# Kernel optimization log

Measured on AMD Instinct MI355X. Metric: run time of the kernel, lower is better.

Reference implementation:

```python
import jax, jax.numpy as jnp
import numpy as np

B, S, HID = 2, 4096, 2048
H, D = 16, 128
BS = 64            # block_size
SR = 0.5           # sparsity_ratio
NB = S // BS       # number of diagonal blocks
SCALE = D ** -0.5


def setup_inputs() -> dict:
    key = jax.random.key(0)
    ks = jax.random.split(key, 7)
    s = 0.02
    return {
        "hidden_states": jax.random.normal(ks[0], (B, S, HID), jnp.float32),
        "Wq": jax.random.normal(ks[1], (HID, H * D), jnp.float32) * s,
        "Wk": jax.random.normal(ks[2], (HID, H * D), jnp.float32) * s,
        "Wv": jax.random.normal(ks[3], (HID, H * D), jnp.float32) * s,
        "Wo": jax.random.normal(ks[4], (H * D, HID), jnp.float32) * s,
        "Wr": jax.random.normal(ks[5], (HID, H), jnp.float32) * s,   # block_router weight
        "br": jax.random.normal(ks[6], (H,), jnp.float32) * s,       # block_router bias
    }


def reference(hidden_states, Wq, Wk, Wv, Wo, Wr, br):
    # projections: torch Linear(x) == x @ W^T; weights stored pre-transposed here
    q = (hidden_states @ Wq).reshape(B, S, H, D).transpose(0, 2, 1, 3)  # [B,H,S,D]
    k = (hidden_states @ Wk).reshape(B, S, H, D).transpose(0, 2, 1, 3)
    v = (hidden_states @ Wv).reshape(B, S, H, D).transpose(0, 2, 1, 3)

    # per-head routing score, mean-pooled over batch (as in torch: routing_scores[:, h].mean())
    routing = jax.nn.sigmoid(hidden_states.mean(axis=1) @ Wr + br)      # [B,H]
    head_score = routing.mean(axis=0)                                   # [H]
    eff_sparsity = SR * (1.0 - head_score * 0.5)
    # torch: max(1, int(block_size * eff)); positive -> floor == int truncation
    attend_count = jnp.maximum(1, jnp.floor(BS * eff_sparsity).astype(jnp.int32))  # [H]

    # block-diagonal attention: only within-block scores are ever finite, so we
    # never materialize the full SxS matrix (softmax over -inf elsewhere is a no-op)
    qb = q.reshape(B, H, NB, BS, D)
    kb = k.reshape(B, H, NB, BS, D)
    vb = v.reshape(B, H, NB, BS, D)
    scores = jnp.einsum("bhnqd,bhnkd->bhnqk", qb, kb) * SCALE           # [B,H,NB,BS,BS]

    # rank of each key within its row (descending); keep == variable-k top-k mask.
    order = jnp.argsort(-scores, axis=-1)
    rank = jnp.argsort(order, axis=-1)
    keep = rank < attend_count[None, :, None, None, None]
    # non-top-k in-block entries are scattered as 0.0 (not -inf) in the original
    masked = jnp.where(keep, scores, 0.0)

    probs = jax.nn.softmax(masked.astype(jnp.float32), axis=-1).astype(q.dtype)
    out_b = jnp.einsum("bhnqk,bhnkd->bhnqd", probs, vb)                 # [B,H,NB,BS,D]
    out = out_b.reshape(B, H, S, D).transpose(0, 2, 1, 3).reshape(B, S, H * D)
    return out @ Wo
```

## Files before the change

### kernel.cpp

```cpp
#include <hip/hip_runtime.h>
#include <hip/hip_bf16.h>
#include <cstdint>
#include <cstddef>

#define B_   2
#define S_   4096
#define HIDN 2048
#define H_   16
#define D_   128
#define NB_  64
#define MTOT 8192
#define QKVN 6144
#define SCALE_ 0.08838834764831845f

typedef unsigned short ushort_t;
typedef __attribute__((ext_vector_type(8))) short short8;
typedef __attribute__((ext_vector_type(8))) ushort_t ushort8;
typedef __attribute__((ext_vector_type(4))) float f32x4;

__device__ inline float b2f(ushort_t x){ union{unsigned u; float f;} v; v.u=((unsigned)x)<<16; return v.f; }
__device__ inline ushort_t f2b(float f){ union{unsigned u; float f;} v; v.f=f; unsigned r=(v.u + 0x7FFF + ((v.u>>16)&1))>>16; return (ushort_t)r; }

#define MFMA_BF16(a,b,c) __builtin_amdgcn_mfma_f32_16x16x32_bf16((a),(b),(c),0,0,0)

__device__ inline void async16(const ushort_t* g, ushort_t* l){
  __builtin_amdgcn_global_load_lds(
      (const __attribute__((address_space(1))) void*)g,
      (__attribute__((address_space(3))) void*)l, 16, 0, 0);
}

__global__ void bsa_convpart(const float* __restrict__ hs, ushort_t* __restrict__ hsB,
                             float* __restrict__ part){
  int t = threadIdx.x;
  int c  = blockIdx.x*512 + t*2;
  int sc = blockIdx.y;
  int b  = blockIdx.z;
  const float* p = hs  + ((size_t)b*S_ + (size_t)sc*128)*HIDN + c;
  ushort_t*    q = hsB + ((size_t)b*S_ + (size_t)sc*128)*HIDN + c;
  float s0=0.f, s1=0.f;
  #pragma unroll 8
  for (int i=0;i<128;i++){
    float2 v = *(const float2*)(p + (size_t)i*HIDN);
    s0 += v.x; s1 += v.y;
    unsigned pk = (unsigned)f2b(v.x) | ((unsigned)f2b(v.y)<<16);
    *(unsigned*)(q + (size_t)i*HIDN) = pk;
  }
  part[((b*32+sc)*HIDN)+c]   = s0;
  part[((b*32+sc)*HIDN)+c+1] = s1;
}

__global__ void bsa_router(const float* __restrict__ part, const float* __restrict__ Wr,
                           const float* __restrict__ br, int* __restrict__ counts){
  __shared__ float cm[2*HIDN];
  __shared__ float sig[2*H_];
  int t = threadIdx.x;
  {
    int b  = t>>9;
    int c4 = (t&511)*4;
    float sx=0.f, sy=0.f, sz=0.f, sw=0.f;
    for (int j=0;j<32;j++){
      float4 v = *(const float4*)&part[((b*32+j)*HIDN)+c4];
      sx+=v.x; sy+=v.y; sz+=v.z; sw+=v.w;
    }
    cm[b*HIDN+c4+0]=sx*(1.0f/S_);
    cm[b*HIDN+c4+1]=sy*(1.0f/S_);
    cm[b*HIDN+c4+2]=sz*(1.0f/S_);
    cm[b*HIDN+c4+3]=sw*(1.0f/S_);
  }
  __syncthreads();
  if (t < 256){
    int g = t>>3;
    int sl = t&7;
    int b = g>>4, h = g&15;
    float acc = 0.f;
    for (int c=sl; c<HIDN; c+=8) acc += cm[b*HIDN+c]*Wr[c*H_+h];
    acc += __shfl_xor(acc, 4);
    acc += __shfl_xor(acc, 2);
    acc += __shfl_xor(acc, 1);
    if (sl==0) sig[g] = 1.f/(1.f+expf(-(acc + br[h])));
  }
  __syncthreads();
  if (t < H_){
    float score = 0.5f*(sig[t] + sig[H_+t]);
    float eff = 0.5f*(1.0f - score*0.5f);
    int ac = (int)floorf(64.f*eff);
    if (ac < 1) ac = 1;
    counts[t] = ac;
  }
}

__global__ void bsa_transpose(const float* w0, const float* w1, const float* w2, const float* w3,
                              ushort_t* o0, ushort_t* o1, ushort_t* o2, ushort_t* o3){
  const float* src; ushort_t* dst;
  switch(blockIdx.z){
    case 0: src=w0; dst=o0; break;
    case 1: src=w1; dst=o1; break;
    case 2: src=w2; dst=o2; break;
    default: src=w3; dst=o3; break;
  }
  __shared__ ushort_t tt[64*72];
  int t = threadIdx.x;
  int r0 = blockIdx.y*64, c0 = blockIdx.x*64;
  #pragma unroll
  for (int it=0; it<16; it++){
    int f = it*256 + t;
    int r = f>>6, c = f&63;
    tt[c*72 + (r ^ ((c&7)<<3))] = f2b(src[(size_t)(r0+r)*HIDN + (c0+c)]);
  }
  __syncthreads();
  #pragma unroll
  for (int it=0; it<2; it++){
    int f = it*256 + t;
    int cc = f>>3, rb = (f&7)<<3;
    ushort8 v = *(const ushort8*)&tt[cc*72 + (rb ^ ((cc&7)<<3))];
    *(ushort8*)&dst[(size_t)(c0+cc)*HIDN + r0 + rb] = v;
  }
}


#define SBAR asm volatile("s_barrier" ::: "memory")
#define WVM4 asm volatile("s_waitcnt vmcnt(4)" ::: "memory")
#define WVM2 asm volatile("s_waitcnt vmcnt(2)" ::: "memory")
#define WVM0 asm volatile("s_waitcnt vmcnt(0)" ::: "memory")
#define PHI  __builtin_amdgcn_s_setprio(1)
#define PLO  __builtin_amdgcn_s_setprio(0)

__device__ __forceinline__ short8 lds_frag(const ushort_t* buf, int row, int kb){
  int off = ((row<<7) + kb) ^ ((row&7)<<4);
  return *(const short8*)((const char*)buf + off);
}

__device__ __forceinline__ void rd_a(short8 (&a)[4][2], const ushort_t* buf, int r0, int l16, int quad){
  #pragma unroll
  for (int mi=0; mi<4; mi++)
    #pragma unroll
    for (int ks=0; ks<2; ks++)
      a[mi][ks] = lds_frag(buf, r0 + mi*16 + l16, ks*64 + quad*16);
}
__device__ __forceinline__ void rd_a2(short8 (&a)[4][2], const ushort_t* buf, int r0, int l16, int quad, int mi0){
  #pragma unroll
  for (int mi=mi0; mi<mi0+2; mi++)
    #pragma unroll
    for (int ks=0; ks<2; ks++)
      a[mi][ks] = lds_frag(buf, r0 + mi*16 + l16, ks*64 + quad*16);
}
__device__ __forceinline__ void rd_b(short8 (&b)[2][2], const ushort_t* buf, int r0, int l16, int quad){
  #pragma unroll
  for (int ni=0; ni<2; ni++)
    #pragma unroll
    for (int ks=0; ks<2; ks++)
      b[ni][ks] = lds_frag(buf, r0 + ni*16 + l16, ks*64 + quad*16);
}
__device__ __forceinline__ void mm8(f32x4 (&acc)[8][4], const short8 (&a)[4][2],
                                    const short8 (&b)[2][2], int mo, int no){
  #pragma unroll
  for (int mi=0; mi<4; mi++)
    #pragma unroll
    for (int ni=0; ni<2; ni++){
      acc[mo+mi][no+ni] = MFMA_BF16(a[mi][0], b[ni][0], acc[mo+mi][no+ni]);
      acc[mo+mi][no+ni] = MFMA_BF16(a[mi][1], b[ni][1], acc[mo+mi][no+ni]);
    }
}
__device__ __forceinline__ void mm8h(f32x4 (&acc)[8][4], const short8 (&a)[4][2],
                                     const short8 (&b)[2][2], int mo, int no, int mi0){
  #pragma unroll
  for (int mi=mi0; mi<mi0+2; mi++)
    #pragma unroll
    for (int ni=0; ni<2; ni++){
      acc[mo+mi][no+ni] = MFMA_BF16(a[mi][0], b[ni][0], acc[mo+mi][no+ni]);
      acc[mo+mi][no+ni] = MFMA_BF16(a[mi][1], b[ni][1], acc[mo+mi][no+ni]);
    }
}
__device__ __forceinline__ void stage_half(ushort_t* ldsHalf, const ushort_t* g,
                                           int K, int w, int roff, int coff){
  async16(g + (size_t)(w*16 + roff)*K + coff,     ldsHalf + (w*2+0)*512);
  async16(g + (size_t)(w*16 + 8 + roff)*K + coff, ldsHalf + (w*2+1)*512);
}

template<int F32OUT>
__global__ __launch_bounds__(512, 2) void bsa_gemm8(const ushort_t* __restrict__ A,
                                                    const ushort_t* __restrict__ BT,
                                                    void* __restrict__ Cv,
                                                    int M, int N, int K){
  extern __shared__ __align__(16) ushort_t sm[];
  ushort_t* A0  = sm;
  ushort_t* A1  = sm + 16384;
  ushort_t* Bb0 = sm + 32768;
  ushort_t* Bb1 = sm + 49152;

  int t = threadIdx.x;
  int w = t>>6, lane = t&63, quad = lane>>4, l16 = lane&15;
  int wr = w>>2, wc = w&3;

  int nbx = N>>8;
  int nwg = (M>>8)*nbx;
  int bid = blockIdx.x;
  int swz = (bid&7)*(nwg>>3) + (bid>>3);
  int bx = swz % nbx, by = swz / nbx;
  int m0 = by<<8, n0 = bx<<8;

  const ushort_t* Ag = A  + (size_t)m0*K;
  const ushort_t* Bg = BT + (size_t)n0*K;
  int roff = lane>>3;
  int coff = ((lane&7) ^ roff) << 3;

  f32x4 acc[8][4] = {};
  short8 a[4][2], b0[2][2], b1[2][2];

  stage_half(A0,        Ag,                      K, w, roff, coff);
  stage_half(A0+8192,   Ag + (size_t)128*K,      K, w, roff, coff);
  stage_half(Bb0,       Bg,                      K, w, roff, coff);
  stage_half(Bb0+8192,  Bg + (size_t)128*K,      K, w, roff, coff);
  stage_half(Bb1,       Bg + 64,                 K, w, roff, coff);
  stage_half(Bb1+8192,  Bg + (size_t)128*K + 64, K, w, roff, coff);
  WVM4;
  SBAR;
  rd_a(a,  A0,  wr*128,    l16, quad);
  rd_b(b0, Bb0, wc*64,     l16, quad);
  rd_b(b1, Bb0, wc*64+32,  l16, quad);

  int nit = K>>7;
  #pragma unroll 1
  for (int i=0; i<nit; i++){
    bool nl = (i+1 < nit);
    int kA  = (2*i+1)<<6;
    int kN0 = (2*i+2)<<6;
    int kN1 = (2*i+3)<<6;
    stage_half(A1, Ag + kA, K, w, roff, coff);
    PHI; mm8(acc, a, b0, 0,0); PLO;
    SBAR;
    stage_half(A1+8192, Ag + (size_t)128*K + kA, K, w, roff, coff);
    PHI;
    mm8h(acc, a, b1, 0,2, 0);
    rd_a2(a, A0, wr*128+64, l16, quad, 0);
    mm8h(acc, a, b1, 0,2, 2);
    rd_a2(a, A0, wr*128+64, l16, quad, 2);
    PLO;
    WVM4;
    SBAR;
    if (nl) stage_half(Bb0, Bg + kN0, K, w, roff, coff);
    PHI; mm8(acc, a, b1, 4,2); PLO;
    rd_b(b1, Bb1, wc*64+32, l16, quad);
    SBAR;
    if (nl) stage_half(Bb0+8192, Bg + (size_t)128*K + kN0, K, w, roff, coff);
    PHI; mm8(acc, a, b0, 4,0); PLO;
    rd_b(b0, Bb1, wc*64, l16, quad);
    if (nl) { WVM4; } else { WVM0; }
    SBAR;
    rd_a(a, A1, wr*128, l16, quad);
    if (nl) stage_half(A0, Ag + kN0, K, w, roff, coff);
    PHI; mm8(acc, a, b0, 0,0); PLO;
    SBAR;
    if (nl) stage_half(A0+8192, Ag + (size_t)128*K + kN0, K, w, roff, coff);
    PHI;
    mm8h(acc, a, b1, 0,2, 0);
    rd_a2(a, A1, wr*128+64, l16, quad, 0);
    mm8h(acc, a, b1, 0,2, 2);
    rd_a2(a, A1, wr*128+64, l16, quad, 2);
    PLO;
    if (nl) { WVM4; }
    SBAR;
    if (nl) stage_half(Bb1, Bg + kN1, K, w, roff, coff);
    PHI; mm8(acc, a, b1, 4,2); PLO;
    if (nl) rd_b(b1, Bb0, wc*64+32, l16, quad);
    if (nl) { WVM2; }
    SBAR;
    if (nl) stage_half(Bb1+8192, Bg + (size_t)128*K + kN1, K, w, roff, coff);
    PHI; mm8(acc, a, b0, 4,0); PLO;
    if (nl){
      rd_b(b0, Bb0, wc*64,  l16, quad);
      rd_a(a,  A0,  wr*128, l16, quad);
    }
    SBAR;
  }

  #pragma unroll
  for (int mi=0; mi<8; mi++)
    #pragma unroll
    for (int ni=0; ni<4; ni++){
      int m = m0 + wr*128 + mi*16 + quad*4;
      int n = n0 + wc*64 + ni*16 + l16;
      #pragma unroll
      for (int r=0;r<4;r++){
        if (F32OUT) ((float*)Cv)[(size_t)(m+r)*N + n] = acc[mi][ni][r];
        else        ((ushort_t*)Cv)[(size_t)(m+r)*N + n] = f2b(acc[mi][ni][r]);
      }
    }
}

__global__ __launch_bounds__(256) void bsa_attn(const ushort_t* __restrict__ QKV,
                                                const int* __restrict__ counts,
                                                ushort_t* __restrict__ O){
  __shared__ __align__(16) ushort_t regA[64*136];
  __shared__ __align__(16) ushort_t regB[64*136];
  __shared__ __align__(16) ushort_t Ps[64*72];
  float* Sc = (float*)regA;

  int t = threadIdx.x, w = t>>6, lane = t&63, quad = lane>>4, l16 = lane&15;
  int bid = blockIdx.x;
  int b  = bid>>10;
  int h  = (bid>>6)&15;
  int nb = bid&63;
  size_t qbase = ((size_t)b*S_ + (size_t)nb*64)*QKVN + (size_t)h*D_;
  size_t obase = ((size_t)b*S_ + (size_t)nb*64)*HIDN + (size_t)h*D_;

  int4 vre[4];
  #pragma unroll
  for (int it=0; it<4; it++){
    int f = it*256 + t;
    int r = f>>4, c = (f&15)*8;
    vre[it] = *(const int4*)(QKV + qbase + 4096 + (size_t)r*QKVN + c);
  }

  #pragma unroll
  for (int it=0; it<4; it++){
    int f = it*256 + t;
    int r = f>>4, c = (f&15)*8;
    *(int4*)(&regA[r*136+c]) = *(const int4*)(QKV + qbase +        (size_t)r*QKVN + c);
    *(int4*)(&regB[r*136+c]) = *(const int4*)(QKV + qbase + 2048 + (size_t)r*QKVN + c);
  }
  __syncthreads();

  f32x4 sacc[4] = {};
  #pragma unroll
  for (int ks=0; ks<4; ks++){
    short8 afr = *(const short8*)(&regA[(w*16 + l16)*136 + ks*32 + quad*8]);
    #pragma unroll
    for (int nt=0; nt<4; nt++){
      short8 bfr = *(const short8*)(&regB[(nt*16 + l16)*136 + ks*32 + quad*8]);
      sacc[nt] = MFMA_BF16(afr, bfr, sacc[nt]);
    }
  }
  __syncthreads();

  #pragma unroll
  for (int nt=0; nt<4; nt++)
    #pragma unroll
    for (int r=0;r<4;r++)
      Sc[(w*16 + quad*4 + r)*68 + nt*16 + l16] = sacc[nt][r]*SCALE_;
  #pragma unroll
  for (int it=0; it<4; it++){
    int f = it*256 + t;
    int r = f>>4, c = (f&15)*8;
    *(int4*)(&regB[r*136+c]) = vre[it];
  }

  int cnt = counts[h];
  for (int g=0; g<4; g++){
    float s[4], v[4];
    #pragma unroll
    for (int rr=0; rr<4; rr++){
      s[rr] = Sc[(w*16 + g*4 + rr)*68 + lane];
      v[rr] = s[rr];
    }
    #pragma unroll
    for (int k=2; k<=64; k<<=1){
      #pragma unroll
      for (int m=k>>1; m>=1; m>>=1){
        #pragma unroll
        for (int rr=0; rr<4; rr++){
          float o = __shfl_xor(v[rr], m);
          bool keepMin = (((lane & k)==0) == ((lane & m)==0));
          float lo = fminf(v[rr], o), hi = fmaxf(v[rr], o);
          v[rr] = keepMin ? lo : hi;
        }
      }
    }
    #pragma unroll
    for (int rr=0; rr<4; rr++){
      float T = __shfl(v[rr], 64 - cnt);
      unsigned long long gt = __ballot(s[rr] > T);
      unsigned long long eq = __ballot(s[rr] == T);
      int G = __popcll(gt);
      int eqr = __popcll(eq & ((1ull<<lane)-1ull));
      bool keep = (s[rr] > T) || ((s[rr] == T) && (eqr < cnt - G));
      float m = keep ? s[rr] : 0.0f;
      float mx = fmaxf(__shfl(v[rr], 63), 0.0f);
      float e = __expf(m - mx);
      float sum = e;
      #pragma unroll
      for (int off=32; off; off>>=1) sum += __shfl_xor(sum, off);
      Ps[(w*16 + g*4 + rr)*72 + lane] = f2b(e/sum);
    }
  }
  __syncthreads();

  f32x4 oacc[4][2] = {};
  #pragma unroll
  for (int ks=0; ks<2; ks++){
    short8 bv[2];
    #pragma unroll
    for (int jj=0; jj<2; jj++){
      int n = (w*2+jj)*16 + l16;
      short8 x;
      #pragma unroll
      for (int j=0;j<8;j++){
        int k = ks*32 + quad*8 + j;
        x[j] = (short)regB[k*136 + n];
      }
      bv[jj] = x;
    }
    #pragma unroll
    for (int mt=0; mt<4; mt++){
      short8 aP = *(const short8*)(&Ps[(mt*16 + l16)*72 + ks*32 + quad*8]);
      #pragma unroll
      for (int jj=0; jj<2; jj++)
        oacc[mt][jj] = MFMA_BF16(aP, bv[jj], oacc[mt][jj]);
    }
  }
  #pragma unroll
  for (int mt=0; mt<4; mt++)
    #pragma unroll
    for (int jj=0; jj<2; jj++){
      int row = mt*16 + quad*4;
      int col = (w*2+jj)*16 + l16;
      #pragma unroll
      for (int r=0;r<4;r++)
        O[obase + (size_t)(row+r)*HIDN + col] = f2b(oacc[mt][jj][r]);
    }
}

extern "C" void kernel_launch(void* const* d_in, const int* in_sizes, int n_in,
                              void* d_out, int out_size, void* d_ws, size_t ws_size,
                              hipStream_t stream) {
  const float* hs = (const float*)d_in[0];
  const float* Wq = (const float*)d_in[1];
  const float* Wk = (const float*)d_in[2];
  const float* Wv = (const float*)d_in[3];
  const float* Wo = (const float*)d_in[4];
  const float* Wr = (const float*)d_in[5];
  const float* br = (const float*)d_in[6];
  float* out = (float*)d_out;
  char* ws = (char*)d_ws;

  const size_t MB = 1024u*1024u;
  float*    part   = (float*)(ws + 0);
  int*      counts = (int*)(ws + 512u*1024u);
  ushort_t* hsB    = (ushort_t*)(ws + 1*MB);
  ushort_t* WqT    = (ushort_t*)(ws + 33*MB);
  ushort_t* WkT    = (ushort_t*)(ws + 41*MB);
  ushort_t* WvT    = (ushort_t*)(ws + 49*MB);
  ushort_t* WoT    = (ushort_t*)(ws + 57*MB);
  ushort_t* QKV    = (ushort_t*)(ws + 65*MB);
  ushort_t* AO     = hsB;

  static bool attr_done = false;
  if (!attr_done){
    hipFuncSetAttribute((const void*)&bsa_gemm8<0>,
                        hipFuncAttributeMaxDynamicSharedMemorySize, 131072);
    hipFuncSetAttribute((const void*)&bsa_gemm8<1>,
                        hipFuncAttributeMaxDynamicSharedMemorySize, 131072);
    attr_done = true;
  }

  bsa_convpart  <<<dim3(4,32,2),  256, 0, stream>>>(hs, hsB, part);
  bsa_router    <<<1,            1024, 0, stream>>>(part, Wr, br, counts);
  bsa_transpose <<<dim3(32,32,4), 256, 0, stream>>>(Wq,Wk,Wv,Wo, WqT,WkT,WvT,WoT);
  bsa_gemm8<0><<<dim3(768), 512, 131072, stream>>>(hsB, WqT, (void*)QKV, MTOT, QKVN, 2048);
  bsa_attn      <<<2048,          256, 0, stream>>>(QKV, counts, AO);
  bsa_gemm8<1><<<dim3(256), 512, 131072, stream>>>(AO, WoT, (void*)out, MTOT, 2048, 2048);
}
```

Measured before the change: 670.6 us.

## Reorder GEMM main loop schedule of LDS fragment reads and async waits

Restructures the double-buffered bf16 GEMM inner loop. It now reads A fragments right before each quarter of MFMAs instead of interleaving half-fragment reads inside the MFMA block, changes the order in which the four accumulator quadrants are computed, and relaxes the vmcnt waits (vmcnt 6/4 instead of 4/2). The aim is to give outstanding global-to-LDS loads more slack and to simplify the LDS read pattern. The cost is that LDS read latency is exposed before MFMA blocks, and the barrier and wait ordering must remain correct for the buffer reuse.

```diff
diff --git a/kernel.cpp b/kernel.cpp
--- a/kernel.cpp
+++ b/kernel.cpp
@@ -119,8 +119,8 @@
 
 
 #define SBAR asm volatile("s_barrier" ::: "memory")
+#define WVM6 asm volatile("s_waitcnt vmcnt(6)" ::: "memory")
 #define WVM4 asm volatile("s_waitcnt vmcnt(4)" ::: "memory")
-#define WVM2 asm volatile("s_waitcnt vmcnt(2)" ::: "memory")
 #define WVM0 asm volatile("s_waitcnt vmcnt(0)" ::: "memory")
 #define PHI  __builtin_amdgcn_s_setprio(1)
 #define PLO  __builtin_amdgcn_s_setprio(0)
@@ -137,13 +137,6 @@
     for (int ks=0; ks<2; ks++)
       a[mi][ks] = lds_frag(buf, r0 + mi*16 + l16, ks*64 + quad*16);
 }
-__device__ __forceinline__ void rd_a2(short8 (&a)[4][2], const ushort_t* buf, int r0, int l16, int quad, int mi0){
-  #pragma unroll
-  for (int mi=mi0; mi<mi0+2; mi++)
-    #pragma unroll
-    for (int ks=0; ks<2; ks++)
-      a[mi][ks] = lds_frag(buf, r0 + mi*16 + l16, ks*64 + quad*16);
-}
 __device__ __forceinline__ void rd_b(short8 (&b)[2][2], const ushort_t* buf, int r0, int l16, int quad){
   #pragma unroll
   for (int ni=0; ni<2; ni++)
@@ -155,16 +148,6 @@
                                     const short8 (&b)[2][2], int mo, int no){
   #pragma unroll
   for (int mi=0; mi<4; mi++)
-    #pragma unroll
-    for (int ni=0; ni<2; ni++){
-      acc[mo+mi][no+ni] = MFMA_BF16(a[mi][0], b[ni][0], acc[mo+mi][no+ni]);
-      acc[mo+mi][no+ni] = MFMA_BF16(a[mi][1], b[ni][1], acc[mo+mi][no+ni]);
-    }
-}
-__device__ __forceinline__ void mm8h(f32x4 (&acc)[8][4], const short8 (&a)[4][2],
-                                     const short8 (&b)[2][2], int mo, int no, int mi0){
-  #pragma unroll
-  for (int mi=mi0; mi<mi0+2; mi++)
     #pragma unroll
     for (int ni=0; ni<2; ni++){
       acc[mo+mi][no+ni] = MFMA_BF16(a[mi][0], b[ni][0], acc[mo+mi][no+ni]);
@@ -215,7 +198,6 @@
   stage_half(Bb1+8192,  Bg + (size_t)128*K + 64, K, w, roff, coff);
   WVM4;
   SBAR;
-  rd_a(a,  A0,  wr*128,    l16, quad);
   rd_b(b0, Bb0, wc*64,     l16, quad);
   rd_b(b1, Bb0, wc*64+32,  l16, quad);
 
@@ -227,49 +209,41 @@
     int kN0 = (2*i+2)<<6;
     int kN1 = (2*i+3)<<6;
     stage_half(A1, Ag + kA, K, w, roff, coff);
+    rd_a(a, A0, wr*128, l16, quad);
     PHI; mm8(acc, a, b0, 0,0); PLO;
     SBAR;
     stage_half(A1+8192, Ag + (size_t)128*K + kA, K, w, roff, coff);
-    PHI;
-    mm8h(acc, a, b1, 0,2, 0);
-    rd_a2(a, A0, wr*128+64, l16, quad, 0);
-    mm8h(acc, a, b1, 0,2, 2);
-    rd_a2(a, A0, wr*128+64, l16, quad, 2);
-    PLO;
-    WVM4;
+    PHI; mm8(acc, a, b1, 0,2); PLO;
+    rd_a(a, A0, wr*128+64, l16, quad);
     SBAR;
     if (nl) stage_half(Bb0, Bg + kN0, K, w, roff, coff);
+    PHI; mm8(acc, a, b0, 4,0); PLO;
+    if (nl) { WVM6; } else { WVM4; }
+    SBAR;
+    if (nl) stage_half(Bb0+8192, Bg + (size_t)128*K + kN0, K, w, roff, coff);
     PHI; mm8(acc, a, b1, 4,2); PLO;
+    if (nl) { WVM4; } else { WVM0; }
+    rd_b(b0, Bb1, wc*64, l16, quad);
+    SBAR;
+    if (nl) stage_half(A0, Ag + kN0, K, w, roff, coff);
+    rd_a(a, A1, wr*128, l16, quad);
     rd_b(b1, Bb1, wc*64+32, l16, quad);
-    SBAR;
-    if (nl) stage_half(Bb0+8192, Bg + (size_t)128*K + kN0, K, w, roff, coff);
+    PHI; mm8(acc, a, b0, 0,0); PLO;
+    SBAR;
+    if (nl) stage_half(A0+8192, Ag + (size_t)128*K + kN0, K, w, roff, coff);
+    PHI; mm8(acc, a, b1, 0,2); PLO;
+    rd_a(a, A1, wr*128+64, l16, quad);
+    SBAR;
+    if (nl) stage_half(Bb1, Bg + kN1, K, w, roff, coff);
     PHI; mm8(acc, a, b0, 4,0); PLO;
-    rd_b(b0, Bb1, wc*64, l16, quad);
-    if (nl) { WVM4; } else { WVM0; }
-    SBAR;
-    rd_a(a, A1, wr*128, l16, quad);
-    if (nl) stage_half(A0, Ag + kN0, K, w, roff, coff);
-    PHI; mm8(acc, a, b0, 0,0); PLO;
-    SBAR;
-    if (nl) stage_half(A0+8192, Ag + (size_t)128*K + kN0, K, w, roff, coff);
-    PHI;
-    mm8h(acc, a, b1, 0,2, 0);
-    rd_a2(a, A1, wr*128+64, l16, quad, 0);
-    mm8h(acc, a, b1, 0,2, 2);
-    rd_a2(a, A1, wr*128+64, l16, quad, 2);
-    PLO;
-    if (nl) { WVM4; }
-    SBAR;
-    if (nl) stage_half(Bb1, Bg + kN1, K, w, roff, coff);
+    if (nl) { WVM6; }
+    SBAR;
+    if (nl) stage_half(Bb1+8192, Bg + (size_t)128*K + kN1, K, w, roff, coff);
     PHI; mm8(acc, a, b1, 4,2); PLO;
-    if (nl) rd_b(b1, Bb0, wc*64+32, l16, quad);
-    if (nl) { WVM2; }
-    SBAR;
-    if (nl) stage_half(Bb1+8192, Bg + (size_t)128*K + kN1, K, w, roff, coff);
-    PHI; mm8(acc, a, b0, 4,0); PLO;
     if (nl){
-      rd_b(b0, Bb0, wc*64,  l16, quad);
-      rd_a(a,  A0,  wr*128, l16, quad);
+      WVM4;
+      rd_b(b0, Bb0, wc*64,    l16, quad);
+      rd_b(b1, Bb0, wc*64+32, l16, quad);
     }
     SBAR;
   }
```

After: 606.5 us. 1.11x faster.
